# Optimization experiments

Measured on AMD Instinct MI355X. Metric: run time of the kernel, lower is better.

Reference implementation:

```python
import jax, jax.numpy as jnp
import numpy as np

N_NODES = 100000
N_ANCHORS = 32
EMB_DIM = 64


def setup_inputs() -> dict:
    key = jax.random.key(0)
    k1, k2, k3, k4, k5 = jax.random.split(key, 5)
    embeds = jax.random.normal(k1, (N_NODES, EMB_DIM), dtype=jnp.float32)
    dists_array = jax.random.uniform(k2, (N_NODES, N_ANCHORS), dtype=jnp.float32)
    # torch Linear(2*D, D): y = x @ W.T + b; we store W already transposed [2D, D]
    W_hidden = jax.random.normal(k3, (2 * EMB_DIM, EMB_DIM), dtype=jnp.float32) * (1.0 / np.sqrt(2 * EMB_DIM))
    b_hidden = jax.random.normal(k4, (EMB_DIM,), dtype=jnp.float32) * 0.01
    anchorset_id = jax.random.randint(k5, (N_ANCHORS,), 0, N_NODES)
    return {
        "embeds": embeds,
        "dists_array": dists_array,
        "W_hidden": W_hidden,
        "b_hidden": b_hidden,
        "anchorset_id": anchorset_id,
    }


def reference(embeds, dists_array, W_hidden, b_hidden, anchorset_id):
    # embeds: [N, D]; dists_array: [N, A]; anchorset_id: [A]
    set_emb = embeds[anchorset_id]                         # gather -> [A, D]
    msg_anchor = dists_array[:, :, None] * set_emb[None]   # [N, A, D]
    self_feat = jnp.broadcast_to(embeds[:, None, :], msg_anchor.shape)  # [N, A, D]
    messages = jnp.concatenate((msg_anchor, self_feat), axis=-1)        # [N, A, 2D]
    hidden = jnp.einsum('nae,ed->nad', messages, W_hidden) + b_hidden   # [N, A, D]
    return hidden.mean(axis=1)                              # [N, D]
```

## Files before the change

kernel.cpp:

```cpp
#include <hip/hip_runtime.h>
#include <cstdint>
#include <cstddef>


#define N_NODES 100000
#define DIM     64
#define NTILES  1563
#define GRIDM   782
#define AS_K    104

typedef short bf16x8 __attribute__((ext_vector_type(8)));
typedef float f32x4  __attribute__((ext_vector_type(4)));

__device__ __forceinline__ unsigned short f2bf(float f) {
    union { float f; unsigned u; } c; c.f = f;
    return (unsigned short)((c.u + 0x7fffu + ((c.u >> 16) & 1u)) >> 16);
}
__device__ __forceinline__ float bf2f(unsigned short h) {
    union { unsigned u; float f; } c; c.u = ((unsigned)h) << 16; return c.f;
}

__global__ __launch_bounds__(256) void pnn_prep(
    const float* __restrict__ embeds, const float* __restrict__ W,
    const int* __restrict__ aid, float* __restrict__ P)
{
    const int t = blockIdx.x * 256 + threadIdx.x;
    const int a = t >> 6, d = t & 63;
    const float* se = embeds + (size_t)aid[a] * DIM;
    float s = 0.f;
    #pragma unroll
    for (int e = 0; e < DIM; ++e) s += se[e] * W[e * DIM + d];
    P[t] = s * (1.0f / 32.0f);
}

__global__ __launch_bounds__(256) void pnn_pack(
    const float* __restrict__ P, const float* __restrict__ W,
    unsigned short* __restrict__ fragB)
{
    const int idx = blockIdx.x * 256 + threadIdx.x;
    const int j  = idx & 7;
    const int ln = (idx >> 3) & 63;
    const int pl = (idx >> 9) & 1;
    const int nt = (idx >> 10) & 3;
    const int ks = idx >> 12;
    const int k  = ks * 32 + (ln >> 4) * 8 + j;
    const int n  = nt * 16 + (ln & 15);
    const float w = (k < 32) ? P[k * 64 + n]
                             : W[(k + 32) * 64 + n];
    unsigned short h = f2bf(w);
    if (pl) h = f2bf(w - bf2f(h));
    fragB[idx] = h;
}

__global__ __launch_bounds__(256, 3) void pnn_main(
    const float* __restrict__ embeds,
    const float* __restrict__ dists,
    const unsigned short* __restrict__ fragB,
    const float* __restrict__ bias,
    float* __restrict__ out)
{
    __shared__ unsigned short As[2][4][16][AS_K];

    const int tid  = threadIdx.x;
    const int wave = tid >> 6;
    const int lane = tid & 63;
    const int quad = lane >> 4;
    const int col  = lane & 15;

    bf16x8 Bf[3][4][2];
    {
        const bf16x8* Bg = (const bf16x8*)fragB;
        #pragma unroll
        for (int ks = 0; ks < 3; ++ks)
            #pragma unroll
            for (int nt = 0; nt < 4; ++nt)
                #pragma unroll
                for (int pl = 0; pl < 2; ++pl)
                    Bf[ks][nt][pl] = Bg[((ks * 4 + nt) * 2 + pl) * 64 + lane];
    }
    float bias_n[4];
    #pragma unroll
    for (int nt = 0; nt < 4; ++nt) bias_n[nt] = bias[nt * 16 + col];

    for (int tile = blockIdx.x; tile < NTILES; tile += GRIDM) {
        const int n0 = tile * 64;

        float4 dv[2], ev[4];
        {
            const float4* dg = (const float4*)(dists + (size_t)n0 * 32);
            #pragma unroll
            for (int i = 0; i < 2; ++i) {
                const int f = i * 256 + tid;
                dv[i] = (n0 + (f >> 3) < N_NODES) ? dg[f] : make_float4(0.f,0.f,0.f,0.f);
            }
            const float4* eg = (const float4*)(embeds + (size_t)n0 * 64);
            #pragma unroll
            for (int i = 0; i < 4; ++i) {
                const int f = i * 256 + tid;
                ev[i] = (n0 + (f >> 4) < N_NODES) ? eg[f] : make_float4(0.f,0.f,0.f,0.f);
            }
        }
        #pragma unroll
        for (int i = 0; i < 2; ++i) {
            const int f  = i * 256 + tid;
            const int nd = f >> 3, k0 = (f & 7) * 4;
            unsigned short* hp = &As[0][nd >> 4][nd & 15][k0];
            unsigned short* lp = &As[1][nd >> 4][nd & 15][k0];
            const float4 v = dv[i];
            unsigned short h0=f2bf(v.x),h1=f2bf(v.y),h2=f2bf(v.z),h3=f2bf(v.w);
            *(unsigned*)hp       = (unsigned)h0 | ((unsigned)h1 << 16);
            *(unsigned*)(hp + 2) = (unsigned)h2 | ((unsigned)h3 << 16);
            unsigned short l0=f2bf(v.x-bf2f(h0)),l1=f2bf(v.y-bf2f(h1)),
                           l2=f2bf(v.z-bf2f(h2)),l3=f2bf(v.w-bf2f(h3));
            *(unsigned*)lp       = (unsigned)l0 | ((unsigned)l1 << 16);
            *(unsigned*)(lp + 2) = (unsigned)l2 | ((unsigned)l3 << 16);
        }
        #pragma unroll
        for (int i = 0; i < 4; ++i) {
            const int f  = i * 256 + tid;
            const int nd = f >> 4, k0 = 32 + (f & 15) * 4;
            unsigned short* hp = &As[0][nd >> 4][nd & 15][k0];
            unsigned short* lp = &As[1][nd >> 4][nd & 15][k0];
            const float4 v = ev[i];
            unsigned short h0=f2bf(v.x),h1=f2bf(v.y),h2=f2bf(v.z),h3=f2bf(v.w);
            *(unsigned*)hp       = (unsigned)h0 | ((unsigned)h1 << 16);
            *(unsigned*)(hp + 2) = (unsigned)h2 | ((unsigned)h3 << 16);
            unsigned short l0=f2bf(v.x-bf2f(h0)),l1=f2bf(v.y-bf2f(h1)),
                           l2=f2bf(v.z-bf2f(h2)),l3=f2bf(v.w-bf2f(h3));
            *(unsigned*)lp       = (unsigned)l0 | ((unsigned)l1 << 16);
            *(unsigned*)(lp + 2) = (unsigned)l2 | ((unsigned)l3 << 16);
        }
        __syncthreads();

        f32x4 acc[4];
        #pragma unroll
        for (int nt = 0; nt < 4; ++nt) {
            const float b = bias_n[nt];
            acc[nt][0] = b; acc[nt][1] = b; acc[nt][2] = b; acc[nt][3] = b;
        }
        #pragma unroll
        for (int ks = 0; ks < 3; ++ks) {
            const bf16x8 Ahi = *(const bf16x8*)&As[0][wave][col][ks * 32 + quad * 8];
            const bf16x8 Alo = *(const bf16x8*)&As[1][wave][col][ks * 32 + quad * 8];
            #pragma unroll
            for (int nt = 0; nt < 4; ++nt) {
                acc[nt] = __builtin_amdgcn_mfma_f32_16x16x32_bf16(Ahi, Bf[ks][nt][0], acc[nt], 0, 0, 0);
                acc[nt] = __builtin_amdgcn_mfma_f32_16x16x32_bf16(Ahi, Bf[ks][nt][1], acc[nt], 0, 0, 0);
                acc[nt] = __builtin_amdgcn_mfma_f32_16x16x32_bf16(Alo, Bf[ks][nt][0], acc[nt], 0, 0, 0);
            }
        }

        #pragma unroll
        for (int r = 0; r < 4; ++r) {
            const int node = n0 + wave * 16 + quad * 4 + r;
            if (node < N_NODES) {
                float* po = out + (size_t)node * DIM + col;
                #pragma unroll
                for (int nt = 0; nt < 4; ++nt) po[nt * 16] = acc[nt][r];
            }
        }
        __syncthreads();
    }
}

extern "C" void kernel_launch(void* const* d_in, const int* in_sizes, int n_in,
                              void* d_out, int out_size, void* d_ws, size_t ws_size,
                              hipStream_t stream) {
    const float* embeds = (const float*)d_in[0];
    const float* dists  = (const float*)d_in[1];
    const float* W      = (const float*)d_in[2];
    const float* bias   = (const float*)d_in[3];
    const int*   aid    = (const int*)d_in[4];
    float* out = (float*)d_out;

    float*          P     = (float*)d_ws;
    unsigned short* fragB = (unsigned short*)((char*)d_ws + 2048 * sizeof(float));

    pnn_prep<<<8, 256, 0, stream>>>(embeds, W, aid, P);
    pnn_pack<<<48, 256, 0, stream>>>(P, W, fragB);
    pnn_main<<<GRIDM, 256, 0, stream>>>(embeds, dists, fragB, bias, out);
}
```

Measured before the change: 102.9 us.

## Merge prep kernels, stage B fragments in LDS, prefetch next tile

Folds the anchor-projection and fragment-packing kernels into a single launch that writes MFMA-ready B fragments directly, removing one kernel launch and the intermediate P buffer. The main kernel now copies the B fragments into shared memory instead of holding them in registers, which frees VGPRs but adds LDS reads inside the MFMA loop. It also register-prefetches the next tile's dists and embeds rows while computing the current tile, and packs bf16 hi/lo values as 64-bit LDS stores. The grid shrinks slightly to 768 blocks.

```diff
diff --git a/kernel.cpp b/kernel.cpp
--- a/kernel.cpp
+++ b/kernel.cpp
@@ -6,7 +6,7 @@
 #define N_NODES 100000
 #define DIM     64
 #define NTILES  1563
-#define GRIDM   782
+#define GRID    768
 #define AS_K    104
 
 typedef short bf16x8 __attribute__((ext_vector_type(8)));
@@ -19,38 +19,70 @@
 __device__ __forceinline__ float bf2f(unsigned short h) {
     union { unsigned u; float f; } c; c.u = ((unsigned)h) << 16; return c.f;
 }
+__device__ __forceinline__ unsigned long long pack4h(float a, float b, float c, float d) {
+    unsigned short h0 = f2bf(a), h1 = f2bf(b), h2 = f2bf(c), h3 = f2bf(d);
+    return (unsigned long long)h0 | ((unsigned long long)h1 << 16) |
+           ((unsigned long long)h2 << 32) | ((unsigned long long)h3 << 48);
+}
+__device__ __forceinline__ unsigned long long pack4l(float a, float b, float c, float d) {
+    unsigned short l0 = f2bf(a - bf2f(f2bf(a))), l1 = f2bf(b - bf2f(f2bf(b)));
+    unsigned short l2 = f2bf(c - bf2f(f2bf(c))), l3 = f2bf(d - bf2f(f2bf(d)));
+    return (unsigned long long)l0 | ((unsigned long long)l1 << 16) |
+           ((unsigned long long)l2 << 32) | ((unsigned long long)l3 << 48);
+}
 
 __global__ __launch_bounds__(256) void pnn_prep(
     const float* __restrict__ embeds, const float* __restrict__ W,
-    const int* __restrict__ aid, float* __restrict__ P)
+    const int* __restrict__ aid, unsigned short* __restrict__ fragB)
 {
-    const int t = blockIdx.x * 256 + threadIdx.x;
-    const int a = t >> 6, d = t & 63;
-    const float* se = embeds + (size_t)aid[a] * DIM;
-    float s = 0.f;
-    #pragma unroll
-    for (int e = 0; e < DIM; ++e) s += se[e] * W[e * DIM + d];
-    P[t] = s * (1.0f / 32.0f);
+    const int b = blockIdx.x, tid = threadIdx.x;
+    if (b < 8) {
+        const int t = b * 256 + tid;
+        const int a = t >> 6, d = t & 63;
+        const float* se = embeds + (size_t)aid[a] * DIM;
+        float s = 0.f;
+        #pragma unroll
+        for (int e = 0; e < DIM; ++e) s += se[e] * W[e * DIM + d];
+        s *= (1.0f / 32.0f);
+        const int j = a & 7, quad = a >> 3;
+        const int nt = d >> 4, col = d & 15;
+        const int lane = quad * 16 + col;
+        const unsigned short hi = f2bf(s);
+        fragB[((nt * 2 + 0) * 64 + lane) * 8 + j] = hi;
+        fragB[((nt * 2 + 1) * 64 + lane) * 8 + j] = f2bf(s - bf2f(hi));
+    } else {
+        const int w = (b - 8) * 256 + tid;
+        const int j    = w & 7;
+        const int lane = (w >> 3) & 63;
+        const int pl   = (w >> 9) & 1;
+        const int nt   = (w >> 10) & 3;
+        const int ks   = 1 + (w >> 12);
+        const int k = ks * 32 + (lane >> 4) * 8 + j;
+        const int n = nt * 16 + (lane & 15);
+        const float v = W[(k + 32) * DIM + n];
+        unsigned short h = f2bf(v);
+        if (pl) h = f2bf(v - bf2f(h));
+        fragB[(((ks * 4 + nt) * 2 + pl) * 64 + lane) * 8 + j] = h;
+    }
 }
 
-__global__ __launch_bounds__(256) void pnn_pack(
-    const float* __restrict__ P, const float* __restrict__ W,
-    unsigned short* __restrict__ fragB)
-{
-    const int idx = blockIdx.x * 256 + threadIdx.x;
-    const int j  = idx & 7;
-    const int ln = (idx >> 3) & 63;
-    const int pl = (idx >> 9) & 1;
-    const int nt = (idx >> 10) & 3;
-    const int ks = idx >> 12;
-    const int k  = ks * 32 + (ln >> 4) * 8 + j;
-    const int n  = nt * 16 + (ln & 15);
-    const float w = (k < 32) ? P[k * 64 + n]
-                             : W[(k + 32) * 64 + n];
-    unsigned short h = f2bf(w);
-    if (pl) h = f2bf(w - bf2f(h));
-    fragB[idx] = h;
-}
+#define LOAD_TILE(m0)                                                          \
+    do {                                                                       \
+        const float4* dg = (const float4*)(dists + (size_t)(m0) * 32);         \
+        _Pragma("unroll")                                                      \
+        for (int i = 0; i < 2; ++i) {                                          \
+            const int f = i * 256 + tid;                                       \
+            dv[i] = ((m0) + (f >> 3) < N_NODES) ? dg[f]                        \
+                                                : make_float4(0.f,0.f,0.f,0.f);\
+        }                                                                      \
+        const float4* eg = (const float4*)(embeds + (size_t)(m0) * 64);        \
+        _Pragma("unroll")                                                      \
+        for (int i = 0; i < 4; ++i) {                                          \
+            const int f = i * 256 + tid;                                       \
+            ev[i] = ((m0) + (f >> 4) < N_NODES) ? eg[f]                        \
+                                                : make_float4(0.f,0.f,0.f,0.f);\
+        }                                                                      \
+    } while (0)
 
 __global__ __launch_bounds__(256, 3) void pnn_main(
     const float* __restrict__ embeds,
@@ -59,7 +91,8 @@
     const float* __restrict__ bias,
     float* __restrict__ out)
 {
-    __shared__ unsigned short As[2][4][16][AS_K];
+    __shared__ __align__(16) unsigned short sB[12288];
+    __shared__ __align__(16) unsigned short As[2][4][16][AS_K];
 
     const int tid  = threadIdx.x;
     const int wave = tid >> 6;
@@ -67,86 +100,62 @@
     const int quad = lane >> 4;
     const int col  = lane & 15;
 
-    bf16x8 Bf[3][4][2];
-    {
-        const bf16x8* Bg = (const bf16x8*)fragB;
-        #pragma unroll
-        for (int ks = 0; ks < 3; ++ks)
-            #pragma unroll
-            for (int nt = 0; nt < 4; ++nt)
-                #pragma unroll
-                for (int pl = 0; pl < 2; ++pl)
-                    Bf[ks][nt][pl] = Bg[((ks * 4 + nt) * 2 + pl) * 64 + lane];
-    }
+    #pragma unroll
+    for (int i = 0; i < 6; ++i)
+        ((uint4*)sB)[i * 256 + tid] = ((const uint4*)fragB)[i * 256 + tid];
+
     float bias_n[4];
     #pragma unroll
     for (int nt = 0; nt < 4; ++nt) bias_n[nt] = bias[nt * 16 + col];
 
-    for (int tile = blockIdx.x; tile < NTILES; tile += GRIDM) {
+    int tile = blockIdx.x;
+    float4 dv[2], ev[4];
+    LOAD_TILE(tile * 64);
+
+    for (; tile < NTILES; tile += GRID) {
         const int n0 = tile * 64;
 
-        float4 dv[2], ev[4];
-        {
-            const float4* dg = (const float4*)(dists + (size_t)n0 * 32);
-            #pragma unroll
-            for (int i = 0; i < 2; ++i) {
-                const int f = i * 256 + tid;
-                dv[i] = (n0 + (f >> 3) < N_NODES) ? dg[f] : make_float4(0.f,0.f,0.f,0.f);
-            }
-            const float4* eg = (const float4*)(embeds + (size_t)n0 * 64);
-            #pragma unroll
-            for (int i = 0; i < 4; ++i) {
-                const int f = i * 256 + tid;
-                ev[i] = (n0 + (f >> 4) < N_NODES) ? eg[f] : make_float4(0.f,0.f,0.f,0.f);
-            }
-        }
         #pragma unroll
         for (int i = 0; i < 2; ++i) {
             const int f  = i * 256 + tid;
             const int nd = f >> 3, k0 = (f & 7) * 4;
-            unsigned short* hp = &As[0][nd >> 4][nd & 15][k0];
-            unsigned short* lp = &As[1][nd >> 4][nd & 15][k0];
             const float4 v = dv[i];
-            unsigned short h0=f2bf(v.x),h1=f2bf(v.y),h2=f2bf(v.z),h3=f2bf(v.w);
-            *(unsigned*)hp       = (unsigned)h0 | ((unsigned)h1 << 16);
-            *(unsigned*)(hp + 2) = (unsigned)h2 | ((unsigned)h3 << 16);
-            unsigned short l0=f2bf(v.x-bf2f(h0)),l1=f2bf(v.y-bf2f(h1)),
-                           l2=f2bf(v.z-bf2f(h2)),l3=f2bf(v.w-bf2f(h3));
-            *(unsigned*)lp       = (unsigned)l0 | ((unsigned)l1 << 16);
-            *(unsigned*)(lp + 2) = (unsigned)l2 | ((unsigned)l3 << 16);
+            *(unsigned long long*)&As[0][nd >> 4][nd & 15][k0] = pack4h(v.x, v.y, v.z, v.w);
+            *(unsigned long long*)&As[1][nd >> 4][nd & 15][k0] = pack4l(v.x, v.y, v.z, v.w);
         }
         #pragma unroll
         for (int i = 0; i < 4; ++i) {
             const int f  = i * 256 + tid;
             const int nd = f >> 4, k0 = 32 + (f & 15) * 4;
-            unsigned short* hp = &As[0][nd >> 4][nd & 15][k0];
-            unsigned short* lp = &As[1][nd >> 4][nd & 15][k0];
             const float4 v = ev[i];
-            unsigned short h0=f2bf(v.x),h1=f2bf(v.y),h2=f2bf(v.z),h3=f2bf(v.w);
-            *(unsigned*)hp       = (unsigned)h0 | ((unsigned)h1 << 16);
-            *(unsigned*)(hp + 2) = (unsigned)h2 | ((unsigned)h3 << 16);
-            unsigned short l0=f2bf(v.x-bf2f(h0)),l1=f2bf(v.y-bf2f(h1)),
-                           l2=f2bf(v.z-bf2f(h2)),l3=f2bf(v.w-bf2f(h3));
-            *(unsigned*)lp       = (unsigned)l0 | ((unsigned)l1 << 16);
-            *(unsigned*)(lp + 2) = (unsigned)l2 | ((unsigned)l3 << 16);
+            *(unsigned long long*)&As[0][nd >> 4][nd & 15][k0] = pack4h(v.x, v.y, v.z, v.w);
+            *(unsigned long long*)&As[1][nd >> 4][nd & 15][k0] = pack4l(v.x, v.y, v.z, v.w);
         }
         __syncthreads();
+
+        const int t2 = tile + GRID;
+        if (t2 < NTILES) {
+            LOAD_TILE(t2 * 64);
+        }
 
         f32x4 acc[4];
         #pragma unroll
         for (int nt = 0; nt < 4; ++nt) {
-            const float b = bias_n[nt];
-            acc[nt][0] = b; acc[nt][1] = b; acc[nt][2] = b; acc[nt][3] = b;
+            const float bb = bias_n[nt];
+            acc[nt][0] = bb; acc[nt][1] = bb; acc[nt][2] = bb; acc[nt][3] = bb;
         }
+        const bf16x8* Bl = (const bf16x8*)sB;
         #pragma unroll
         for (int ks = 0; ks < 3; ++ks) {
             const bf16x8 Ahi = *(const bf16x8*)&As[0][wave][col][ks * 32 + quad * 8];
             const bf16x8 Alo = *(const bf16x8*)&As[1][wave][col][ks * 32 + quad * 8];
             #pragma unroll
             for (int nt = 0; nt < 4; ++nt) {
-                acc[nt] = __builtin_amdgcn_mfma_f32_16x16x32_bf16(Ahi, Bf[ks][nt][0], acc[nt], 0, 0, 0);
-                acc[nt] = __builtin_amdgcn_mfma_f32_16x16x32_bf16(Ahi, Bf[ks][nt][1], acc[nt], 0, 0, 0);
-                acc[nt] = __builtin_amdgcn_mfma_f32_16x16x32_bf16(Alo, Bf[ks][nt][0], acc[nt], 0, 0, 0);
+                const bf16x8 Bh = Bl[((ks * 4 + nt) * 2 + 0) * 64 + lane];
+                const bf16x8 Bo = Bl[((ks * 4 + nt) * 2 + 1) * 64 + lane];
+                acc[nt] = __builtin_amdgcn_mfma_f32_16x16x32_bf16(Ahi, Bh, acc[nt], 0, 0, 0);
+                acc[nt] = __builtin_amdgcn_mfma_f32_16x16x32_bf16(Ahi, Bo, acc[nt], 0, 0, 0);
+                acc[nt] = __builtin_amdgcn_mfma_f32_16x16x32_bf16(Alo, Bh, acc[nt], 0, 0, 0);
             }
         }
 
@@ -173,10 +182,8 @@
     const int*   aid    = (const int*)d_in[4];
     float* out = (float*)d_out;
 
-    float*          P     = (float*)d_ws;
-    unsigned short* fragB = (unsigned short*)((char*)d_ws + 2048 * sizeof(float));
+    unsigned short* fragB = (unsigned short*)d_ws;
 
-    pnn_prep<<<8, 256, 0, stream>>>(embeds, W, aid, P);
-    pnn_pack<<<48, 256, 0, stream>>>(P, W, fragB);
-    pnn_main<<<GRIDM, 256, 0, stream>>>(embeds, dists, fragB, bias, out);
+    pnn_prep<<<40, 256, 0, stream>>>(embeds, W, aid, fragB);
+    pnn_main<<<GRID, 256, 0, stream>>>(embeds, dists, fragB, bias, out);
 }
```

Measured after the change: 94.14 us. 8.5% less time.
